# Kernel optimization log

Hardware: AMD Instinct MI355X
Metric: run time of the kernel (lower is better)

Reference implementation:

```python
import jax, jax.numpy as jnp
import numpy as np

N, E = 50000, 1600000
D_IN, D_HID, D_OUT = 256, 256, 128  # 2*output_dim = 256, output_dim = 128


def glorot(key, shape):
    fan_in, fan_out = shape
    limit = np.sqrt(6.0 / (fan_in + fan_out)).astype(np.float32)
    return jax.random.uniform(key, shape, jnp.float32, -limit, limit)


def setup_inputs() -> dict:
    key = jax.random.key(0)
    k0, k1, k2, k3 = jax.random.split(key, 4)
    x = jax.random.normal(k0, (N, D_IN), jnp.float32)
    edge_index = jax.random.randint(k1, (2, E), 0, N, jnp.int32)
    W1 = glorot(k2, (D_IN, D_HID))
    b1 = jnp.zeros((D_HID,), jnp.float32)
    W2 = glorot(k3, (D_HID, D_OUT))
    b2 = jnp.zeros((D_OUT,), jnp.float32)
    return {"x": x, "edge_index": edge_index, "W1": W1, "b1": b1, "W2": W2, "b2": b2}


def gcn_propagate(x, src, dst, num_nodes):
    """One hop of D^-1/2 (A + I) D^-1/2 @ x (PyG gcn_norm with self-loops)."""
    loops = jnp.arange(num_nodes, dtype=src.dtype)
    src_sl = jnp.concatenate([src, loops])  # [E + N]
    dst_sl = jnp.concatenate([dst, loops])
    ones = jnp.ones(src_sl.shape, x.dtype)
    deg = jax.ops.segment_sum(ones, dst_sl, num_segments=num_nodes)  # >= 1 (self-loop)
    dinv = jax.lax.rsqrt(jnp.maximum(deg, 1e-12))
    norm = dinv[src_sl] * dinv[dst_sl]  # [E + N]
    msgs = x[src_sl] * norm[:, None]    # gather + scale, [E+N, D]
    return jax.ops.segment_sum(msgs, dst_sl, num_segments=num_nodes)


def reference(x, edge_index, W1, b1, W2, b2):
    src, dst = edge_index[0], edge_index[1]
    n = x.shape[0]
    # SGConv(K=1): propagate then linear. conv1 + ReLU
    h = jax.nn.relu(gcn_propagate(x, src, dst, n) @ W1 + b1)
    # conv2 (GAE branch)
    return gcn_propagate(h, src, dst, n) @ W2 + b2
```

## Files before the change

### kernel.cpp

```cpp
#include <hip/hip_runtime.h>

typedef short s16x8 __attribute__((ext_vector_type(8)));
typedef float f32x4 __attribute__((ext_vector_type(4)));
typedef float f32x2 __attribute__((ext_vector_type(2)));

#define TILE 2048

__device__ __forceinline__ unsigned int brne(float f) {
    unsigned int u = __float_as_uint(f);
    return (u + 0x7FFFu + ((u >> 16) & 1u)) >> 16;
}
__device__ __forceinline__ float blo(unsigned int u) { return __uint_as_float(u << 16); }
__device__ __forceinline__ float bhi(unsigned int u) { return __uint_as_float(u & 0xFFFF0000u); }

__device__ __forceinline__ void acc8(float* a, const uint4 u, const float wt) {
    a[0] += blo(u.x) * wt; a[1] += bhi(u.x) * wt;
    a[2] += blo(u.y) * wt; a[3] += bhi(u.y) * wt;
    a[4] += blo(u.z) * wt; a[5] += bhi(u.z) * wt;
    a[6] += blo(u.w) * wt; a[7] += bhi(u.w) * wt;
}

__device__ __forceinline__ unsigned int enc_fp8(float v) {
    return __builtin_amdgcn_cvt_pk_fp8_f32(v, v, 0, false) & 0xFF;
}
__device__ __forceinline__ void dec4(float* f, unsigned int u) {
    f32x2 lo = __builtin_amdgcn_cvt_pk_f32_fp8((int)u, false);
    f32x2 hi = __builtin_amdgcn_cvt_pk_f32_fp8((int)u, true);
    f[0] = lo[0]; f[1] = lo[1]; f[2] = hi[0]; f[3] = hi[1];
}
__device__ __forceinline__ void acc16(float* a, const uint4 u, const float wt) {
    float f[4];
    dec4(f, u.x); a[0] += f[0]*wt; a[1] += f[1]*wt; a[2]  += f[2]*wt; a[3]  += f[3]*wt;
    dec4(f, u.y); a[4] += f[0]*wt; a[5] += f[1]*wt; a[6]  += f[2]*wt; a[7]  += f[3]*wt;
    dec4(f, u.z); a[8] += f[0]*wt; a[9] += f[1]*wt; a[10] += f[2]*wt; a[11] += f[3]*wt;
    dec4(f, u.w); a[12]+= f[0]*wt; a[13]+= f[1]*wt; a[14] += f[2]*wt; a[15] += f[3]*wt;
}


__global__ void k_bhist(const int* __restrict__ dst, int* __restrict__ bucket_cnt,
                        int e, int nb) {
    __shared__ int h[256];
    const int tid = threadIdx.x;
    h[tid] = 0;
    __syncthreads();
    const int base = blockIdx.x * TILE + tid;
#pragma unroll
    for (int k = 0; k < 8; k++) {
        const int i = base + k * 256;
        if (i < e) atomicAdd(&h[dst[i] >> 8], 1);
    }
    __syncthreads();
    if (tid < nb && h[tid]) atomicAdd(&bucket_cnt[tid], h[tid]);
}

__global__ void k_bscan(const int* __restrict__ bucket_cnt, int* __restrict__ bucket_base,
                        int* __restrict__ bucket_cursor, int nb, int e) {
    __shared__ int sh[256];
    const int tid = threadIdx.x;
    const int v = (tid < nb) ? bucket_cnt[tid] : 0;
    int x = v;
    sh[tid] = x;
    __syncthreads();
    for (int off = 1; off < 256; off <<= 1) {
        const int t = (tid >= off) ? sh[tid - off] : 0;
        __syncthreads();
        if (tid >= off) { x += t; sh[tid] = x; }
        __syncthreads();
    }
    if (tid < nb) { bucket_base[tid] = x - v; bucket_cursor[tid] = x - v; }
    if (tid == 0) bucket_base[nb] = e;
}

__global__ void k_bscatter(const int* __restrict__ src, const int* __restrict__ dst,
                           int* __restrict__ bucket_cursor, uint2* __restrict__ eb, int e) {
    __shared__ int h[256], hbase[256], h2[256];
    const int tid = threadIdx.x;
    h[tid] = 0; h2[tid] = 0;
    __syncthreads();
    const int base = blockIdx.x * TILE + tid;
    int s[8], d[8], b[8];
    bool val[8];
#pragma unroll
    for (int k = 0; k < 8; k++) {
        const int i = base + k * 256;
        val[k] = i < e;
        if (val[k]) {
            s[k] = src[i]; d[k] = dst[i]; b[k] = d[k] >> 8;
            atomicAdd(&h[b[k]], 1);
        }
    }
    __syncthreads();
    if (h[tid]) hbase[tid] = atomicAdd(&bucket_cursor[tid], h[tid]);
    __syncthreads();
#pragma unroll
    for (int k = 0; k < 8; k++) {
        if (val[k]) {
            const int off = atomicAdd(&h2[b[k]], 1);
            eb[hbase[b[k]] + off] = make_uint2((unsigned)s[k], (unsigned)d[k]);
        }
    }
}

__global__ void k_nhist(const uint2* __restrict__ eb, const int* __restrict__ bucket_base,
                        int* __restrict__ cnt, float* __restrict__ dinv, int n) {
    __shared__ int c[256];
    const int tid = threadIdx.x, b = blockIdx.x;
    c[tid] = 0;
    __syncthreads();
    const int beg = bucket_base[b], end = bucket_base[b + 1];
    for (int i = beg + tid; i < end; i += 256)
        atomicAdd(&c[eb[i].y & 255], 1);
    __syncthreads();
    const int node = b * 256 + tid;
    if (node < n) {
        cnt[node] = c[tid];
        dinv[node] = rsqrtf((float)(c[tid] + 1));
    }
}

__global__ void k_scan1(const int* __restrict__ cnt, int* __restrict__ rowptr,
                        int* __restrict__ part, int n) {
    __shared__ int sh[256];
    int tid = threadIdx.x;
    int i = blockIdx.x * 256 + tid;
    int v = (i < n) ? cnt[i] : 0;
    int x = v;
    sh[tid] = x;
    __syncthreads();
    for (int off = 1; off < 256; off <<= 1) {
        int t = (tid >= off) ? sh[tid - off] : 0;
        __syncthreads();
        if (tid >= off) { x += t; sh[tid] = x; }
        __syncthreads();
    }
    if (i < n) rowptr[i] = x - v;
    if (tid == 255) part[blockIdx.x] = x;
}

__global__ void k_scan2(int* __restrict__ part, int nb) {
    __shared__ int sh[256];
    int tid = threadIdx.x;
    int v = (tid < nb) ? part[tid] : 0;
    int x = v;
    sh[tid] = x;
    __syncthreads();
    for (int off = 1; off < 256; off <<= 1) {
        int t = (tid >= off) ? sh[tid - off] : 0;
        __syncthreads();
        if (tid >= off) { x += t; sh[tid] = x; }
        __syncthreads();
    }
    if (tid < nb) part[tid] = x - v;
}

__global__ void k_scan3(int* __restrict__ rowptr, const int* __restrict__ part,
                        int n, int e) {
    int i = blockIdx.x * blockDim.x + threadIdx.x;
    if (i < n) rowptr[i] = rowptr[i] + part[i >> 8];
    if (i == 0) rowptr[n] = e;
}

__global__ void k_place(const uint2* __restrict__ eb, const int* __restrict__ bucket_base,
                        const int* __restrict__ rowptr, int* __restrict__ es, int n) {
    __shared__ int offs[256];
    const int tid = threadIdx.x, b = blockIdx.x;
    offs[tid] = 0;
    __syncthreads();
    const int beg = bucket_base[b], end = bucket_base[b + 1];
    for (int i = beg + tid; i < end; i += 256) {
        const uint2 ed = eb[i];
        const int d = (int)ed.y;
        const int local = atomicAdd(&offs[d & 255], 1);
        es[rowptr[d] + local] = (int)ed.x;
    }
}

__global__ void k_cast_x(const float* __restrict__ x, unsigned int* __restrict__ xb2,
                         int total4) {
    int i = blockIdx.x * blockDim.x + threadIdx.x;
    if (i >= total4) return;
    float4 v = ((const float4*)x)[i];
    uint2 p;
    p.x = brne(v.x) | (brne(v.y) << 16);
    p.y = brne(v.z) | (brne(v.w) << 16);
    ((uint2*)xb2)[i] = p;
}

__global__ void k_tW(const float* __restrict__ W, unsigned short* __restrict__ Wt,
                     int total, int nshift) {
    int t = blockIdx.x * blockDim.x + threadIdx.x;
    if (t >= total) return;
    int k = t >> nshift;
    int nn = t & ((1 << nshift) - 1);
    Wt[(size_t)nn * 256 + k] = (unsigned short)brne(W[t]);
}

#define LP 40
template <bool FP8OUT>
__global__ __launch_bounds__(256) void k_gemm_bf16(const unsigned short* __restrict__ A,
                                                   const unsigned short* __restrict__ Bt,
                                                   void* __restrict__ Cout,
                                                   int M, int Nc) {
    __shared__ unsigned short As[128 * LP];
    __shared__ unsigned short Bs[128 * LP];

    const int tid = threadIdx.x;
    const int wave = tid >> 6, lane = tid & 63;
    const int wm = (wave >> 1) * 64, wn = (wave & 1) * 64;
    const int l15 = lane & 15, quad = lane >> 4;
    const int mBase = blockIdx.x * 128, nBase = blockIdx.y * 128;

    f32x4 acc[4][4];
#pragma unroll
    for (int i = 0; i < 4; i++)
#pragma unroll
        for (int j = 0; j < 4; j++) acc[i][j] = (f32x4){0.f, 0.f, 0.f, 0.f};

    const int c0 = tid, c1 = 256 + tid;
    const int r0 = c0 >> 2, kc0 = c0 & 3;
    const int r1 = c1 >> 2, kc1 = c1 & 3;
    int am0 = mBase + r0; if (am0 >= M) am0 = M - 1;
    int am1 = mBase + r1; if (am1 >= M) am1 = M - 1;
    const uint4* Ap0 = (const uint4*)A + (size_t)am0 * 32 + kc0;
    const uint4* Ap1 = (const uint4*)A + (size_t)am1 * 32 + kc1;
    const uint4* Bp0 = (const uint4*)Bt + (size_t)(nBase + r0) * 32 + kc0;
    const uint4* Bp1 = (const uint4*)Bt + (size_t)(nBase + r1) * 32 + kc1;

    for (int kt = 0; kt < 8; ++kt) {
        uint4 a0 = Ap0[kt * 4];
        uint4 a1 = Ap1[kt * 4];
        uint4 b0 = Bp0[kt * 4];
        uint4 b1 = Bp1[kt * 4];
        __syncthreads();
        *(uint4*)&As[r0 * LP + kc0 * 8] = a0;
        *(uint4*)&As[r1 * LP + kc1 * 8] = a1;
        *(uint4*)&Bs[r0 * LP + kc0 * 8] = b0;
        *(uint4*)&Bs[r1 * LP + kc1 * 8] = b1;
        __syncthreads();

        s16x8 af[4], bf[4];
#pragma unroll
        for (int i = 0; i < 4; i++)
            af[i] = *(const s16x8*)&As[(wm + i * 16 + l15) * LP + quad * 8];
#pragma unroll
        for (int j = 0; j < 4; j++)
            bf[j] = *(const s16x8*)&Bs[(wn + j * 16 + l15) * LP + quad * 8];
#pragma unroll
        for (int i = 0; i < 4; i++)
#pragma unroll
            for (int j = 0; j < 4; j++)
                acc[i][j] = __builtin_amdgcn_mfma_f32_16x16x32_bf16(af[i], bf[j], acc[i][j], 0, 0, 0);
    }

#pragma unroll
    for (int i = 0; i < 4; i++) {
        const int rowb = mBase + wm + i * 16 + quad * 4;
#pragma unroll
        for (int r = 0; r < 4; r++) {
            const int row = rowb + r;
            if (row < M) {
#pragma unroll
                for (int j = 0; j < 4; j++) {
                    const int col = nBase + wn + j * 16 + l15;
                    if (FP8OUT)
                        ((unsigned char*)Cout)[(size_t)row * Nc + col] =
                            (unsigned char)enc_fp8(acc[i][j][r]);
                    else
                        ((unsigned short*)Cout)[(size_t)row * Nc + col] =
                            (unsigned short)brne(acc[i][j][r]);
                }
            }
        }
    }
}

__global__ void k_prop256f8(const uint4* __restrict__ X4,
                            const int* __restrict__ rowptr,
                            const int* __restrict__ es,
                            const float* __restrict__ dinv,
                            const float* __restrict__ bias,
                            uint4* __restrict__ Y4, int n) {
    const int wid = (int)((blockIdx.x * blockDim.x + threadIdx.x) >> 6);
    const int lane = threadIdx.x & 63;
    const int quad = lane >> 4, l16 = lane & 15;
    if (wid >= n) return;
    const float dd = dinv[wid];
    float a[16];
#pragma unroll
    for (int k = 0; k < 16; k++) a[k] = 0.f;
    {
        const uint4 v = X4[(size_t)wid * 16 + l16];
        if (quad == 0) acc16(a, v, dd * dd);
    }
    const int beg = rowptr[wid], end = rowptr[wid + 1];
    int j = beg + quad;
    for (; j + 4 < end; j += 8) {
        const int s0 = es[j], s1 = es[j + 4];
        const float w0 = dinv[s0] * dd, w1 = dinv[s1] * dd;
        const uint4 u0 = X4[(size_t)s0 * 16 + l16];
        const uint4 u1 = X4[(size_t)s1 * 16 + l16];
        acc16(a, u0, w0);
        acc16(a, u1, w1);
    }
    if (j < end) {
        const int s0 = es[j];
        const float w0 = dinv[s0] * dd;
        const uint4 u0 = X4[(size_t)s0 * 16 + l16];
        acc16(a, u0, w0);
    }
#pragma unroll
    for (int k = 0; k < 16; k++) {
        a[k] += __shfl_xor(a[k], 16);
        a[k] += __shfl_xor(a[k], 32);
    }
    if (quad == 0) {
        const float4* bp = (const float4*)bias + l16 * 4;
#pragma unroll
        for (int q = 0; q < 4; q++) {
            const float4 b = bp[q];
            a[q * 4 + 0] = fmaxf(a[q * 4 + 0] + b.x, 0.f);
            a[q * 4 + 1] = fmaxf(a[q * 4 + 1] + b.y, 0.f);
            a[q * 4 + 2] = fmaxf(a[q * 4 + 2] + b.z, 0.f);
            a[q * 4 + 3] = fmaxf(a[q * 4 + 3] + b.w, 0.f);
        }
        uint4 p0, p1;
        p0.x = brne(a[0])  | (brne(a[1])  << 16);
        p0.y = brne(a[2])  | (brne(a[3])  << 16);
        p0.z = brne(a[4])  | (brne(a[5])  << 16);
        p0.w = brne(a[6])  | (brne(a[7])  << 16);
        p1.x = brne(a[8])  | (brne(a[9])  << 16);
        p1.y = brne(a[10]) | (brne(a[11]) << 16);
        p1.z = brne(a[12]) | (brne(a[13]) << 16);
        p1.w = brne(a[14]) | (brne(a[15]) << 16);
        Y4[(size_t)wid * 32 + l16 * 2] = p0;
        Y4[(size_t)wid * 32 + l16 * 2 + 1] = p1;
    }
}

__global__ void k_prop128b(const uint4* __restrict__ X4,
                           const int* __restrict__ rowptr,
                           const int* __restrict__ es,
                           const float* __restrict__ dinv,
                           const float* __restrict__ bias,
                           float* __restrict__ Yout, int n) {
    const int wid = (int)((blockIdx.x * blockDim.x + threadIdx.x) >> 6);
    const int lane = threadIdx.x & 63;
    const int quad = lane >> 4, l16 = lane & 15;
    if (wid >= n) return;
    const float dd = dinv[wid];
    float a[8];
#pragma unroll
    for (int k = 0; k < 8; k++) a[k] = 0.f;
    {
        const uint4 v = X4[(size_t)wid * 16 + l16];
        if (quad == 0) acc8(a, v, dd * dd);
    }
    const int beg = rowptr[wid], end = rowptr[wid + 1];
    int j = beg + quad;
    for (; j + 4 < end; j += 8) {
        const int s0 = es[j], s1 = es[j + 4];
        const float w0 = dinv[s0] * dd, w1 = dinv[s1] * dd;
        const uint4 u0 = X4[(size_t)s0 * 16 + l16];
        const uint4 u1 = X4[(size_t)s1 * 16 + l16];
        acc8(a, u0, w0);
        acc8(a, u1, w1);
    }
    if (j < end) {
        const int s0 = es[j];
        const float w0 = dinv[s0] * dd;
        const uint4 u0 = X4[(size_t)s0 * 16 + l16];
        acc8(a, u0, w0);
    }
#pragma unroll
    for (int k = 0; k < 8; k++) {
        a[k] += __shfl_xor(a[k], 16);
        a[k] += __shfl_xor(a[k], 32);
    }
    if (quad == 0) {
        const float4 b0 = ((const float4*)bias)[l16 * 2];
        const float4 b1 = ((const float4*)bias)[l16 * 2 + 1];
        float4* op = (float4*)Yout + (size_t)wid * 32 + l16 * 2;
        op[0] = make_float4(a[0] + b0.x, a[1] + b0.y, a[2] + b0.z, a[3] + b0.w);
        op[1] = make_float4(a[4] + b1.x, a[5] + b1.y, a[6] + b1.z, a[7] + b1.w);
    }
}

extern "C" void kernel_launch(void* const* d_in, const int* in_sizes, int n_in,
                              void* d_out, int out_size, void* d_ws, size_t ws_size,
                              hipStream_t stream) {
    const float* x  = (const float*)d_in[0];
    const int*   ei = (const int*)d_in[1];
    const float* W1 = (const float*)d_in[2];
    const float* b1 = (const float*)d_in[3];
    const float* W2 = (const float*)d_in[4];
    const float* b2 = (const float*)d_in[5];
    float* out = (float*)d_out;

    const int n = in_sizes[0] / 256;
    const int e = in_sizes[1] / 2;
    const int* src = ei;
    const int* dst = ei + e;
    const int nb = (n + 255) >> 8;

    char* wsp = (char*)d_ws;
    size_t off = 0;
    auto alloc = [&](size_t bytes) -> char* {
        char* p = wsp + off;
        off += (bytes + 511) & ~(size_t)511;
        return p;
    };
    int*   cnt     = (int*)alloc(sizeof(int) * n);
    float* dinv    = (float*)alloc(sizeof(float) * n);
    int*   rowptr  = (int*)alloc(sizeof(int) * (n + 1));
    int*   part    = (int*)alloc(sizeof(int) * 256);
    int*   bcnt    = (int*)alloc(sizeof(int) * 256);
    int*   bbase   = (int*)alloc(sizeof(int) * 257);
    int*   bcur    = (int*)alloc(sizeof(int) * 256);
    int*   es      = (int*)alloc(sizeof(int) * e);
    unsigned short* xb  = (unsigned short*)alloc(2ull * n * 256);
    unsigned short* W1t = (unsigned short*)alloc(2ull * 256 * 256);
    unsigned short* W2t = (unsigned short*)alloc(2ull * 128 * 256);
    unsigned char*  T1  = (unsigned char*)alloc((size_t)n * 256);
    unsigned short* H   = (unsigned short*)alloc(2ull * n * 256);
    unsigned short* T2  = (unsigned short*)alloc(2ull * n * 128);
    uint2* eb = (uint2*)H;

    const int nb_n = (n + 255) / 256;
    const int nb_t = (e + TILE - 1) / TILE;

    (void)hipMemsetAsync(bcnt, 0, sizeof(int) * 256, stream);
    k_bhist<<<nb_t, 256, 0, stream>>>(dst, bcnt, e, nb);
    k_bscan<<<1, 256, 0, stream>>>(bcnt, bbase, bcur, nb, e);
    k_bscatter<<<nb_t, 256, 0, stream>>>(src, dst, bcur, eb, e);
    k_nhist<<<nb, 256, 0, stream>>>(eb, bbase, cnt, dinv, n);
    k_scan1<<<nb_n, 256, 0, stream>>>(cnt, rowptr, part, n);
    k_scan2<<<1, 256, 0, stream>>>(part, nb_n);
    k_scan3<<<nb_n, 256, 0, stream>>>(rowptr, part, n, e);
    k_place<<<nb, 256, 0, stream>>>(eb, bbase, rowptr, es, n);

    const int total4 = n * 256 / 4;
    k_cast_x<<<(total4 + 255) / 256, 256, 0, stream>>>(x, (unsigned int*)xb, total4);
    k_tW<<<(256 * 256 + 255) / 256, 256, 0, stream>>>(W1, W1t, 256 * 256, 8);
    k_tW<<<(256 * 128 + 255) / 256, 256, 0, stream>>>(W2, W2t, 256 * 128, 7);

    dim3 g1((n + 127) / 128, 2);
    k_gemm_bf16<true><<<g1, 256, 0, stream>>>(xb, W1t, T1, n, 256);
    k_prop256f8<<<(n + 3) / 4, 256, 0, stream>>>((const uint4*)T1, rowptr, es,
                                                 dinv, b1, (uint4*)H, n);

    dim3 g2((n + 127) / 128, 1);
    k_gemm_bf16<false><<<g2, 256, 0, stream>>>(H, W2t, T2, n, 128);
    k_prop128b<<<(n + 3) / 4, 256, 0, stream>>>((const uint4*)T2, rowptr, es,
                                                dinv, b2, out, n);
}
```

Before: 337.0 us.

## Fuse x bf16 cast into GEMM, merge scan kernels, pack fp8 decode

The first GEMM now reads the fp32 x directly and converts it to bf16 on load, so the separate cast kernel and its bf16 copy of x are no longer needed. The node histogram is merged with the per-block scan, and the top-level scan is folded into the placement kernel, which cuts the launch count. The two weight transposes become a single kernel. The fp8 propagation accumulates with packed float2 math. In exchange, the GEMM loads twice as many bytes of A per tile and every column block re-reads and re-converts the fp32 rows, and each placement block redoes the small top-level scan.

```diff
diff --git a/kernel.cpp b/kernel.cpp
--- a/kernel.cpp
+++ b/kernel.cpp
@@ -23,17 +23,15 @@
 __device__ __forceinline__ unsigned int enc_fp8(float v) {
     return __builtin_amdgcn_cvt_pk_fp8_f32(v, v, 0, false) & 0xFF;
 }
-__device__ __forceinline__ void dec4(float* f, unsigned int u) {
-    f32x2 lo = __builtin_amdgcn_cvt_pk_f32_fp8((int)u, false);
-    f32x2 hi = __builtin_amdgcn_cvt_pk_f32_fp8((int)u, true);
-    f[0] = lo[0]; f[1] = lo[1]; f[2] = hi[0]; f[3] = hi[1];
-}
-__device__ __forceinline__ void acc16(float* a, const uint4 u, const float wt) {
-    float f[4];
-    dec4(f, u.x); a[0] += f[0]*wt; a[1] += f[1]*wt; a[2]  += f[2]*wt; a[3]  += f[3]*wt;
-    dec4(f, u.y); a[4] += f[0]*wt; a[5] += f[1]*wt; a[6]  += f[2]*wt; a[7]  += f[3]*wt;
-    dec4(f, u.z); a[8] += f[0]*wt; a[9] += f[1]*wt; a[10] += f[2]*wt; a[11] += f[3]*wt;
-    dec4(f, u.w); a[12]+= f[0]*wt; a[13]+= f[1]*wt; a[14] += f[2]*wt; a[15] += f[3]*wt;
+__device__ __forceinline__ void acc16p(f32x2* a, const uint4 u, const f32x2 w2) {
+    a[0] += __builtin_amdgcn_cvt_pk_f32_fp8((int)u.x, false) * w2;
+    a[1] += __builtin_amdgcn_cvt_pk_f32_fp8((int)u.x, true)  * w2;
+    a[2] += __builtin_amdgcn_cvt_pk_f32_fp8((int)u.y, false) * w2;
+    a[3] += __builtin_amdgcn_cvt_pk_f32_fp8((int)u.y, true)  * w2;
+    a[4] += __builtin_amdgcn_cvt_pk_f32_fp8((int)u.z, false) * w2;
+    a[5] += __builtin_amdgcn_cvt_pk_f32_fp8((int)u.z, true)  * w2;
+    a[6] += __builtin_amdgcn_cvt_pk_f32_fp8((int)u.w, false) * w2;
+    a[7] += __builtin_amdgcn_cvt_pk_f32_fp8((int)u.w, true)  * w2;
 }
 
 
@@ -101,9 +99,10 @@
     }
 }
 
-__global__ void k_nhist(const uint2* __restrict__ eb, const int* __restrict__ bucket_base,
-                        int* __restrict__ cnt, float* __restrict__ dinv, int n) {
-    __shared__ int c[256];
+__global__ void k_nhist_scan(const uint2* __restrict__ eb, const int* __restrict__ bucket_base,
+                             int* __restrict__ rowptr, int* __restrict__ part,
+                             float* __restrict__ dinv, int n) {
+    __shared__ int c[256], sh[256];
     const int tid = threadIdx.x, b = blockIdx.x;
     c[tid] = 0;
     __syncthreads();
@@ -111,96 +110,74 @@
     for (int i = beg + tid; i < end; i += 256)
         atomicAdd(&c[eb[i].y & 255], 1);
     __syncthreads();
+    const int v = c[tid];
     const int node = b * 256 + tid;
-    if (node < n) {
-        cnt[node] = c[tid];
-        dinv[node] = rsqrtf((float)(c[tid] + 1));
-    }
-}
-
-__global__ void k_scan1(const int* __restrict__ cnt, int* __restrict__ rowptr,
-                        int* __restrict__ part, int n) {
-    __shared__ int sh[256];
-    int tid = threadIdx.x;
-    int i = blockIdx.x * 256 + tid;
-    int v = (i < n) ? cnt[i] : 0;
+    if (node < n) dinv[node] = rsqrtf((float)(v + 1));
     int x = v;
     sh[tid] = x;
     __syncthreads();
     for (int off = 1; off < 256; off <<= 1) {
-        int t = (tid >= off) ? sh[tid - off] : 0;
+        const int t = (tid >= off) ? sh[tid - off] : 0;
         __syncthreads();
         if (tid >= off) { x += t; sh[tid] = x; }
         __syncthreads();
     }
-    if (i < n) rowptr[i] = x - v;
-    if (tid == 255) part[blockIdx.x] = x;
-}
-
-__global__ void k_scan2(int* __restrict__ part, int nb) {
-    __shared__ int sh[256];
-    int tid = threadIdx.x;
-    int v = (tid < nb) ? part[tid] : 0;
-    int x = v;
+    if (node <= n) rowptr[node] = x - v;
+    if (tid == 255) part[b] = x;
+}
+
+__global__ void k_place(const uint2* __restrict__ eb, const int* __restrict__ bucket_base,
+                        int* __restrict__ rowptr, const int* __restrict__ part,
+                        int* __restrict__ es, int n, int nb) {
+    __shared__ int sh[256], rp[256], offs[256];
+    const int tid = threadIdx.x, b = blockIdx.x;
+    int x = (tid < nb) ? part[tid] : 0;
     sh[tid] = x;
     __syncthreads();
     for (int off = 1; off < 256; off <<= 1) {
-        int t = (tid >= off) ? sh[tid - off] : 0;
+        const int t = (tid >= off) ? sh[tid - off] : 0;
         __syncthreads();
         if (tid >= off) { x += t; sh[tid] = x; }
         __syncthreads();
     }
-    if (tid < nb) part[tid] = x - v;
-}
-
-__global__ void k_scan3(int* __restrict__ rowptr, const int* __restrict__ part,
-                        int n, int e) {
-    int i = blockIdx.x * blockDim.x + threadIdx.x;
-    if (i < n) rowptr[i] = rowptr[i] + part[i >> 8];
-    if (i == 0) rowptr[n] = e;
-}
-
-__global__ void k_place(const uint2* __restrict__ eb, const int* __restrict__ bucket_base,
-                        const int* __restrict__ rowptr, int* __restrict__ es, int n) {
-    __shared__ int offs[256];
-    const int tid = threadIdx.x, b = blockIdx.x;
+    const int prefix = (b > 0) ? sh[b - 1] : 0;
+    const int node = b * 256 + tid;
+    int rg = 0;
+    if (node <= n) {
+        rg = rowptr[node] + prefix;
+        rowptr[node] = rg;
+    }
+    rp[tid] = rg;
     offs[tid] = 0;
     __syncthreads();
     const int beg = bucket_base[b], end = bucket_base[b + 1];
     for (int i = beg + tid; i < end; i += 256) {
         const uint2 ed = eb[i];
-        const int d = (int)ed.y;
-        const int local = atomicAdd(&offs[d & 255], 1);
-        es[rowptr[d] + local] = (int)ed.x;
-    }
-}
-
-__global__ void k_cast_x(const float* __restrict__ x, unsigned int* __restrict__ xb2,
-                         int total4) {
-    int i = blockIdx.x * blockDim.x + threadIdx.x;
-    if (i >= total4) return;
-    float4 v = ((const float4*)x)[i];
-    uint2 p;
-    p.x = brne(v.x) | (brne(v.y) << 16);
-    p.y = brne(v.z) | (brne(v.w) << 16);
-    ((uint2*)xb2)[i] = p;
-}
-
-__global__ void k_tW(const float* __restrict__ W, unsigned short* __restrict__ Wt,
-                     int total, int nshift) {
-    int t = blockIdx.x * blockDim.x + threadIdx.x;
-    if (t >= total) return;
-    int k = t >> nshift;
-    int nn = t & ((1 << nshift) - 1);
-    Wt[(size_t)nn * 256 + k] = (unsigned short)brne(W[t]);
+        const int d = (int)ed.y & 255;
+        const int local = atomicAdd(&offs[d], 1);
+        es[rp[d] + local] = (int)ed.x;
+    }
+}
+
+__global__ void k_tW2(const float* __restrict__ W1, const float* __restrict__ W2,
+                      unsigned short* __restrict__ W1t, unsigned short* __restrict__ W2t) {
+    const int t = blockIdx.x * 256 + threadIdx.x;
+    if (t < 65536) {
+        const int k = t >> 8, nn = t & 255;
+        W1t[nn * 256 + k] = (unsigned short)brne(W1[t]);
+    } else {
+        const int u = t - 65536;
+        const int k = u >> 7, nn = u & 127;
+        W2t[nn * 256 + k] = (unsigned short)brne(W2[u]);
+    }
 }
 
 #define LP 40
-template <bool FP8OUT>
-__global__ __launch_bounds__(256) void k_gemm_bf16(const unsigned short* __restrict__ A,
-                                                   const unsigned short* __restrict__ Bt,
-                                                   void* __restrict__ Cout,
-                                                   int M, int Nc) {
+template <bool AF32, bool FP8OUT>
+__global__ __launch_bounds__(256) void k_gemm(const void* __restrict__ Av,
+                                              const unsigned short* __restrict__ Bt,
+                                              void* __restrict__ Cout,
+                                              int M, int Nc) {
     __shared__ unsigned short As[128 * LP];
     __shared__ unsigned short Bs[128 * LP];
 
@@ -216,26 +193,41 @@
 #pragma unroll
         for (int j = 0; j < 4; j++) acc[i][j] = (f32x4){0.f, 0.f, 0.f, 0.f};
 
-    const int c0 = tid, c1 = 256 + tid;
-    const int r0 = c0 >> 2, kc0 = c0 & 3;
-    const int r1 = c1 >> 2, kc1 = c1 & 3;
-    int am0 = mBase + r0; if (am0 >= M) am0 = M - 1;
-    int am1 = mBase + r1; if (am1 >= M) am1 = M - 1;
-    const uint4* Ap0 = (const uint4*)A + (size_t)am0 * 32 + kc0;
-    const uint4* Ap1 = (const uint4*)A + (size_t)am1 * 32 + kc1;
+    const int r0 = tid >> 2, kc0 = tid & 3;
+    int am0 = mBase + r0;      if (am0 >= M) am0 = M - 1;
+    int am1 = mBase + r0 + 64; if (am1 >= M) am1 = M - 1;
+
+    const uint4* Ap0; const uint4* Ap1; const float4* Af0; const float4* Af1;
+    if (AF32) {
+        Af0 = (const float4*)Av + (size_t)am0 * 64 + kc0 * 2;
+        Af1 = (const float4*)Av + (size_t)am1 * 64 + kc0 * 2;
+    } else {
+        Ap0 = (const uint4*)Av + (size_t)am0 * 32 + kc0;
+        Ap1 = (const uint4*)Av + (size_t)am1 * 32 + kc0;
+    }
     const uint4* Bp0 = (const uint4*)Bt + (size_t)(nBase + r0) * 32 + kc0;
-    const uint4* Bp1 = (const uint4*)Bt + (size_t)(nBase + r1) * 32 + kc1;
+    const uint4* Bp1 = (const uint4*)Bt + (size_t)(nBase + r0 + 64) * 32 + kc0;
 
     for (int kt = 0; kt < 8; ++kt) {
-        uint4 a0 = Ap0[kt * 4];
-        uint4 a1 = Ap1[kt * 4];
-        uint4 b0 = Bp0[kt * 4];
-        uint4 b1 = Bp1[kt * 4];
+        uint4 a0, a1;
+        if (AF32) {
+            const float4 l0 = Af0[kt * 8], h0 = Af0[kt * 8 + 1];
+            const float4 l1 = Af1[kt * 8], h1 = Af1[kt * 8 + 1];
+            a0.x = brne(l0.x) | (brne(l0.y) << 16); a0.y = brne(l0.z) | (brne(l0.w) << 16);
+            a0.z = brne(h0.x) | (brne(h0.y) << 16); a0.w = brne(h0.z) | (brne(h0.w) << 16);
+            a1.x = brne(l1.x) | (brne(l1.y) << 16); a1.y = brne(l1.z) | (brne(l1.w) << 16);
+            a1.z = brne(h1.x) | (brne(h1.y) << 16); a1.w = brne(h1.z) | (brne(h1.w) << 16);
+        } else {
+            a0 = Ap0[kt * 4];
+            a1 = Ap1[kt * 4];
+        }
+        const uint4 b0 = Bp0[kt * 4];
+        const uint4 b1 = Bp1[kt * 4];
         __syncthreads();
         *(uint4*)&As[r0 * LP + kc0 * 8] = a0;
-        *(uint4*)&As[r1 * LP + kc1 * 8] = a1;
+        *(uint4*)&As[(r0 + 64) * LP + kc0 * 8] = a1;
         *(uint4*)&Bs[r0 * LP + kc0 * 8] = b0;
-        *(uint4*)&Bs[r1 * LP + kc1 * 8] = b1;
+        *(uint4*)&Bs[(r0 + 64) * LP + kc0 * 8] = b1;
         __syncthreads();
 
         s16x8 af[4], bf[4];
@@ -285,12 +277,12 @@
     const int quad = lane >> 4, l16 = lane & 15;
     if (wid >= n) return;
     const float dd = dinv[wid];
-    float a[16];
-#pragma unroll
-    for (int k = 0; k < 16; k++) a[k] = 0.f;
+    f32x2 a[8];
+#pragma unroll
+    for (int k = 0; k < 8; k++) a[k] = (f32x2){0.f, 0.f};
     {
         const uint4 v = X4[(size_t)wid * 16 + l16];
-        if (quad == 0) acc16(a, v, dd * dd);
+        if (quad == 0) acc16p(a, v, (f32x2){dd * dd, dd * dd});
     }
     const int beg = rowptr[wid], end = rowptr[wid + 1];
     int j = beg + quad;
@@ -299,39 +291,41 @@
         const float w0 = dinv[s0] * dd, w1 = dinv[s1] * dd;
         const uint4 u0 = X4[(size_t)s0 * 16 + l16];
         const uint4 u1 = X4[(size_t)s1 * 16 + l16];
-        acc16(a, u0, w0);
-        acc16(a, u1, w1);
+        acc16p(a, u0, (f32x2){w0, w0});
+        acc16p(a, u1, (f32x2){w1, w1});
     }
     if (j < end) {
         const int s0 = es[j];
         const float w0 = dinv[s0] * dd;
         const uint4 u0 = X4[(size_t)s0 * 16 + l16];
-        acc16(a, u0, w0);
-    }
-#pragma unroll
-    for (int k = 0; k < 16; k++) {
-        a[k] += __shfl_xor(a[k], 16);
-        a[k] += __shfl_xor(a[k], 32);
+        acc16p(a, u0, (f32x2){w0, w0});
+    }
+#pragma unroll
+    for (int k = 0; k < 8; k++) {
+        a[k][0] += __shfl_xor(a[k][0], 16);
+        a[k][1] += __shfl_xor(a[k][1], 16);
+        a[k][0] += __shfl_xor(a[k][0], 32);
+        a[k][1] += __shfl_xor(a[k][1], 32);
     }
     if (quad == 0) {
         const float4* bp = (const float4*)bias + l16 * 4;
 #pragma unroll
         for (int q = 0; q < 4; q++) {
             const float4 b = bp[q];
-            a[q * 4 + 0] = fmaxf(a[q * 4 + 0] + b.x, 0.f);
-            a[q * 4 + 1] = fmaxf(a[q * 4 + 1] + b.y, 0.f);
-            a[q * 4 + 2] = fmaxf(a[q * 4 + 2] + b.z, 0.f);
-            a[q * 4 + 3] = fmaxf(a[q * 4 + 3] + b.w, 0.f);
+            a[2 * q][0]     = fmaxf(a[2 * q][0] + b.x, 0.f);
+            a[2 * q][1]     = fmaxf(a[2 * q][1] + b.y, 0.f);
+            a[2 * q + 1][0] = fmaxf(a[2 * q + 1][0] + b.z, 0.f);
+            a[2 * q + 1][1] = fmaxf(a[2 * q + 1][1] + b.w, 0.f);
         }
         uint4 p0, p1;
-        p0.x = brne(a[0])  | (brne(a[1])  << 16);
-        p0.y = brne(a[2])  | (brne(a[3])  << 16);
-        p0.z = brne(a[4])  | (brne(a[5])  << 16);
-        p0.w = brne(a[6])  | (brne(a[7])  << 16);
-        p1.x = brne(a[8])  | (brne(a[9])  << 16);
-        p1.y = brne(a[10]) | (brne(a[11]) << 16);
-        p1.z = brne(a[12]) | (brne(a[13]) << 16);
-        p1.w = brne(a[14]) | (brne(a[15]) << 16);
+        p0.x = brne(a[0][0]) | (brne(a[0][1]) << 16);
+        p0.y = brne(a[1][0]) | (brne(a[1][1]) << 16);
+        p0.z = brne(a[2][0]) | (brne(a[2][1]) << 16);
+        p0.w = brne(a[3][0]) | (brne(a[3][1]) << 16);
+        p1.x = brne(a[4][0]) | (brne(a[4][1]) << 16);
+        p1.y = brne(a[5][0]) | (brne(a[5][1]) << 16);
+        p1.z = brne(a[6][0]) | (brne(a[6][1]) << 16);
+        p1.w = brne(a[7][0]) | (brne(a[7][1]) << 16);
         Y4[(size_t)wid * 32 + l16 * 2] = p0;
         Y4[(size_t)wid * 32 + l16 * 2 + 1] = p1;
     }
@@ -409,7 +403,6 @@
         off += (bytes + 511) & ~(size_t)511;
         return p;
     };
-    int*   cnt     = (int*)alloc(sizeof(int) * n);
     float* dinv    = (float*)alloc(sizeof(float) * n);
     int*   rowptr  = (int*)alloc(sizeof(int) * (n + 1));
     int*   part    = (int*)alloc(sizeof(int) * 256);
@@ -417,7 +410,6 @@
     int*   bbase   = (int*)alloc(sizeof(int) * 257);
     int*   bcur    = (int*)alloc(sizeof(int) * 256);
     int*   es      = (int*)alloc(sizeof(int) * e);
-    unsigned short* xb  = (unsigned short*)alloc(2ull * n * 256);
     unsigned short* W1t = (unsigned short*)alloc(2ull * 256 * 256);
     unsigned short* W2t = (unsigned short*)alloc(2ull * 128 * 256);
     unsigned char*  T1  = (unsigned char*)alloc((size_t)n * 256);
@@ -425,31 +417,24 @@
     unsigned short* T2  = (unsigned short*)alloc(2ull * n * 128);
     uint2* eb = (uint2*)H;
 
-    const int nb_n = (n + 255) / 256;
     const int nb_t = (e + TILE - 1) / TILE;
 
     (void)hipMemsetAsync(bcnt, 0, sizeof(int) * 256, stream);
     k_bhist<<<nb_t, 256, 0, stream>>>(dst, bcnt, e, nb);
     k_bscan<<<1, 256, 0, stream>>>(bcnt, bbase, bcur, nb, e);
     k_bscatter<<<nb_t, 256, 0, stream>>>(src, dst, bcur, eb, e);
-    k_nhist<<<nb, 256, 0, stream>>>(eb, bbase, cnt, dinv, n);
-    k_scan1<<<nb_n, 256, 0, stream>>>(cnt, rowptr, part, n);
-    k_scan2<<<1, 256, 0, stream>>>(part, nb_n);
-    k_scan3<<<nb_n, 256, 0, stream>>>(rowptr, part, n, e);
-    k_place<<<nb, 256, 0, stream>>>(eb, bbase, rowptr, es, n);
-
-    const int total4 = n * 256 / 4;
-    k_cast_x<<<(total4 + 255) / 256, 256, 0, stream>>>(x, (unsigned int*)xb, total4);
-    k_tW<<<(256 * 256 + 255) / 256, 256, 0, stream>>>(W1, W1t, 256 * 256, 8);
-    k_tW<<<(256 * 128 + 255) / 256, 256, 0, stream>>>(W2, W2t, 256 * 128, 7);
+    k_nhist_scan<<<nb, 256, 0, stream>>>(eb, bbase, rowptr, part, dinv, n);
+    k_place<<<nb, 256, 0, stream>>>(eb, bbase, rowptr, part, es, n, nb);
+
+    k_tW2<<<(65536 + 32768) / 256, 256, 0, stream>>>(W1, W2, W1t, W2t);
 
     dim3 g1((n + 127) / 128, 2);
-    k_gemm_bf16<true><<<g1, 256, 0, stream>>>(xb, W1t, T1, n, 256);
+    k_gemm<true, true><<<g1, 256, 0, stream>>>(x, W1t, T1, n, 256);
     k_prop256f8<<<(n + 3) / 4, 256, 0, stream>>>((const uint4*)T1, rowptr, es,
                                                  dinv, b1, (uint4*)H, n);
 
     dim3 g2((n + 127) / 128, 1);
-    k_gemm_bf16<false><<<g2, 256, 0, stream>>>(H, W2t, T2, n, 128);
+    k_gemm<false, false><<<g2, 256, 0, stream>>>(H, W2t, T2, n, 128);
     k_prop128b<<<(n + 3) / 4, 256, 0, stream>>>((const uint4*)T2, rowptr, es,
                                                 dinv, b2, out, n);
 }
```

New measurement: 317.7 us. -5.7%, faster.
